# Kernel optimization log

Measured on AMD Instinct MI355X. Metric: run time of the kernel, lower is better.

The kernel has to match this reference:

```python
import jax, jax.numpy as jnp
import numpy as np

DIM = 128
BATCH = 262144
N_PAIRS = DIM * (DIM - 1) // 2  # 8128

# Static pair ordering exactly as in the torch module: (i, j) for i in range(dim) for j in range(i+1, dim)
_p = np.array([(i, j) for i in range(DIM) for j in range(i + 1, DIM)], dtype=np.int32)
I_IDX = jnp.asarray(_p[:, 0])
J_IDX = jnp.asarray(_p[:, 1])


def setup_inputs() -> dict:
    key = jax.random.key(0)
    k1, k2 = jax.random.split(key)
    x = jax.random.normal(k1, (BATCH, DIM), dtype=jnp.float32)
    angles = jax.random.normal(k2, (N_PAIRS,), dtype=jnp.float32) * 0.01
    bias = jnp.zeros((DIM,), dtype=jnp.float32)
    return {"x": x, "angles": angles, "bias": bias}


def _rotation_matrix(angles):
    # The layer is linear: applying the ordered Givens sweep to every row of x
    # equals x @ W where W is the sweep applied to eye(dim) (cf. weight_matrix()).
    # Building W via a scan over the 8128 rotations is the efficient faithful form.
    cos, sin = jnp.cos(angles), jnp.sin(angles)

    def step(W, vals):
        i, j, c, s = vals
        wi = W[:, i]  # [dim]
        wj = W[:, j]
        # out[:, [i,j]] @ [[c, -s], [s, c]]  ->  new_i = wi*c + wj*s ; new_j = wj*c - wi*s
        W = W.at[:, i].set(wi * c + wj * s)
        W = W.at[:, j].set(wj * c - wi * s)
        return W, None

    W0 = jnp.eye(DIM, dtype=angles.dtype)
    W, _ = jax.lax.scan(step, W0, (I_IDX, J_IDX, cos, sin))
    return W


def reference(x, angles, bias):
    W = _rotation_matrix(angles)  # [dim, dim] orthogonal
    return x @ W + bias
```

## Files before the change

kernel.cpp:

```cpp
#include <hip/hip_runtime.h>

typedef float  floatx4  __attribute__((ext_vector_type(4)));
typedef short  bf16x8   __attribute__((ext_vector_type(8)));
typedef float  facc4    __attribute__((ext_vector_type(4)));

__device__ __forceinline__ unsigned short f2bf(float f) {
  unsigned u = __builtin_bit_cast(unsigned, f);
  u = u + 0x7fffu + ((u >> 16) & 1u);
  return (unsigned short)(u >> 16);
}

template <int I0, int I1>
__device__ void gen_chunk(const float* __restrict__ ang, float* __restrict__ out,
                          float* lcs, int tid) {
  constexpr int P0 = I0 * 127 - I0 * (I0 - 1) / 2;
  constexpr int P1 = I1 * 127 - I1 * (I1 - 1) / 2;
  constexpr int NROT = P1 - P0;
  for (int idx = tid; idx < NROT; idx += 256) {
    float s, c;
    sincosf(ang[P0 + idx], &s, &c);
    lcs[2 * idx] = c;
    lcs[2 * idx + 1] = s;
  }
  __syncthreads();
  if (tid >= 128) return;
  float w[128];
#pragma unroll
  for (int k = 0; k < 128; ++k) w[k] = (k == tid) ? 1.0f : 0.0f;
#pragma unroll
  for (int i = I0; i < I1; ++i) {
    float wi = w[i];
#pragma unroll
    for (int j = i + 1; j < 128; ++j) {
      const int p = (i * 127 - (i * (i - 1)) / 2 + (j - i - 1)) - P0;
      const float2 cs2 = *(const float2*)(&lcs[2 * p]);
      const float c = cs2.x, s = cs2.y;
      const float wj = w[j];
      w[j] = fmaf(wj, c, -(wi * s));
      wi   = fmaf(wj, s, wi * c);
    }
    w[i] = wi;
  }
  floatx4* o = (floatx4*)(out + (size_t)tid * 128);
#pragma unroll
  for (int k = 0; k < 32; ++k) {
    floatx4 v;
    v[0] = w[4 * k]; v[1] = w[4 * k + 1]; v[2] = w[4 * k + 2]; v[3] = w[4 * k + 3];
    o[k] = v;
  }
}

__global__ __launch_bounds__(256) void k_wgen(const float* __restrict__ ang,
                                              float* __restrict__ out) {
  __shared__ float lcs[2144];
  const int tid = threadIdx.x;
  switch (blockIdx.x) {
    case 0:  gen_chunk<0,   8>(ang, out + 0 * 16384, lcs, tid); break;
    case 1:  gen_chunk<8,  17>(ang, out + 1 * 16384, lcs, tid); break;
    case 2:  gen_chunk<17, 27>(ang, out + 2 * 16384, lcs, tid); break;
    case 3:  gen_chunk<27, 37>(ang, out + 3 * 16384, lcs, tid); break;
    case 4:  gen_chunk<37, 49>(ang, out + 4 * 16384, lcs, tid); break;
    case 5:  gen_chunk<49, 64>(ang, out + 5 * 16384, lcs, tid); break;
    case 6:  gen_chunk<64, 82>(ang, out + 6 * 16384, lcs, tid); break;
    default: gen_chunk<82, 127>(ang, out + 7 * 16384, lcs, tid); break;
  }
}

__global__ __launch_bounds__(128) void k_combine(const float* __restrict__ chunks,
                                                 unsigned short* __restrict__ wt) {
  __shared__ float sv[128];
  const int r = blockIdx.x;
  const int t = threadIdx.x;
  float v = chunks[r * 128 + t];
  for (int m = 1; m < 8; ++m) {
    __syncthreads();
    sv[t] = v;
    __syncthreads();
    const float* Cm = chunks + m * 16384 + t;
    float a0 = 0.f, a1 = 0.f, a2 = 0.f, a3 = 0.f;
#pragma unroll
    for (int k = 0; k < 128; k += 4) {
      a0 = fmaf(sv[k],     Cm[(k)     * 128], a0);
      a1 = fmaf(sv[k + 1], Cm[(k + 1) * 128], a1);
      a2 = fmaf(sv[k + 2], Cm[(k + 2) * 128], a2);
      a3 = fmaf(sv[k + 3], Cm[(k + 3) * 128], a3);
    }
    v = (a0 + a1) + (a2 + a3);
  }
  wt[t * 136 + r] = f2bf(v);
}

__global__ __launch_bounds__(256) void k_gemm(const float* __restrict__ x,
                                              const unsigned short* __restrict__ wt,
                                              const float* __restrict__ bias,
                                              float* __restrict__ y) {
  __shared__ unsigned short sW[128 * 136];
  __shared__ float sB[128];
  const int tid = threadIdx.x;
  {
    const floatx4* src = (const floatx4*)wt;
    floatx4* dst = (floatx4*)sW;
#pragma unroll
    for (int i2 = 0; i2 < 9; ++i2) {
      int idx = tid + i2 * 256;
      if (idx < 2176) dst[idx] = src[idx];
    }
    if (tid < 128) sB[tid] = bias[tid];
  }
  __syncthreads();

  const int wave = tid >> 6, lane = tid & 63;
  const int m16 = lane & 15, h = lane >> 4;

  const size_t row0 = (size_t)blockIdx.x * 256 + wave * 64 + m16;
  const float* xr0 = x + row0 * 128;
  float* yr0 = y + row0 * 128;

  floatx4 a[8];
#pragma unroll
  for (int c = 0; c < 4; ++c) {
    a[2 * c]     = *(const floatx4*)(xr0 + c * 32 + h * 8);
    a[2 * c + 1] = *(const floatx4*)(xr0 + c * 32 + h * 8 + 4);
  }

#pragma unroll
  for (int it = 0; it < 4; ++it) {
    bf16x8 af[4];
#pragma unroll
    for (int c = 0; c < 4; ++c) {
#pragma unroll
      for (int q = 0; q < 8; ++q) {
        const float f = (q < 4) ? a[2 * c][q] : a[2 * c + 1][q - 4];
        af[c][q] = (short)f2bf(f);
      }
    }
    if (it < 3) {
      const float* xr = xr0 + (size_t)(it + 1) * 16 * 128;
#pragma unroll
      for (int c = 0; c < 4; ++c) {
        a[2 * c]     = *(const floatx4*)(xr + c * 32 + h * 8);
        a[2 * c + 1] = *(const floatx4*)(xr + c * 32 + h * 8 + 4);
      }
    }
    facc4 acc[8];
#pragma unroll
    for (int t = 0; t < 8; ++t) acc[t] = *(const facc4*)(sB + t * 16 + h * 4);
#pragma unroll
    for (int c = 0; c < 4; ++c) {
#pragma unroll
      for (int t = 0; t < 8; ++t) {
        const bf16x8 bw = *(const bf16x8*)(&sW[(t * 16 + m16) * 136 + c * 32 + h * 8]);
        acc[t] = __builtin_amdgcn_mfma_f32_16x16x32_bf16(bw, af[c], acc[t], 0, 0, 0);
      }
    }
    float* yr = yr0 + (size_t)it * 16 * 128;
#pragma unroll
    for (int t = 0; t < 8; ++t) {
      *(floatx4*)(yr + t * 16 + h * 4) = acc[t];
    }
  }
}

extern "C" void kernel_launch(void* const* d_in, const int* in_sizes, int n_in,
                              void* d_out, int out_size, void* d_ws, size_t ws_size,
                              hipStream_t stream) {
  const float* x    = (const float*)d_in[0];
  const float* ang  = (const float*)d_in[1];
  const float* bias = (const float*)d_in[2];
  float* y = (float*)d_out;

  char* ws = (char*)d_ws;
  float* chunks      = (float*)ws;
  unsigned short* wt = (unsigned short*)(ws + 524288);

  k_wgen   <<<8,    256, 0, stream>>>(ang, chunks);
  k_combine<<<128,  128, 0, stream>>>(chunks, wt);
  k_gemm   <<<1024, 256, 0, stream>>>(x, wt, bias, y);
}
```

Baseline: 287.7 us.

## Restructure GEMM: register-resident W slices, shared bf16 X tiles, staged coalesced stores

Each wave now keeps its 32-column slice of W in registers and reuses it across 16 row tiles. X tiles are loaded coalesced, converted to bf16 and placed in a double-buffered, XOR-swizzled shared buffer with global prefetch two tiles ahead. Outputs go through a swizzled shared transpose so global stores are coalesced. This removes the per-block 34KB W copy into shared memory and the strided per-lane X loads, at the cost of a block-wide barrier per tile.

```diff
diff --git a/kernel.cpp b/kernel.cpp
--- a/kernel.cpp
+++ b/kernel.cpp
@@ -3,6 +3,7 @@
 typedef float  floatx4  __attribute__((ext_vector_type(4)));
 typedef short  bf16x8   __attribute__((ext_vector_type(8)));
 typedef float  facc4    __attribute__((ext_vector_type(4)));
+typedef unsigned short ushortx4 __attribute__((ext_vector_type(4)));
 
 __device__ __forceinline__ unsigned short f2bf(float f) {
   unsigned u = __builtin_bit_cast(unsigned, f);
@@ -90,74 +91,102 @@
   wt[t * 136 + r] = f2bf(v);
 }
 
-__global__ __launch_bounds__(256) void k_gemm(const float* __restrict__ x,
-                                              const unsigned short* __restrict__ wt,
-                                              const float* __restrict__ bias,
-                                              float* __restrict__ y) {
-  __shared__ unsigned short sW[128 * 136];
-  __shared__ float sB[128];
+__global__ __launch_bounds__(256, 4) void k_gemm(const float* __restrict__ x,
+                                                 const unsigned short* __restrict__ wt,
+                                                 const float* __restrict__ bias,
+                                                 float* __restrict__ y) {
+  __shared__ unsigned short sX[2][2048];
+  __shared__ float sT[4][512];
+
   const int tid = threadIdx.x;
+  const int wv = tid >> 6, lane = tid & 63;
+  const int m16 = lane & 15, h = lane >> 4;
+
+  bf16x8 bw[2][4];
+#pragma unroll
+  for (int t = 0; t < 2; ++t)
+#pragma unroll
+    for (int c = 0; c < 4; ++c)
+      bw[t][c] = *(const bf16x8*)(wt + (size_t)(wv * 32 + t * 16 + m16) * 136
+                                     + c * 32 + h * 8);
+  facc4 bfr[2];
+#pragma unroll
+  for (int t = 0; t < 2; ++t)
+    bfr[t] = *(const facc4*)(bias + wv * 32 + t * 16 + h * 4);
+
+  const float* xb = x + (size_t)blockIdx.x * 256 * 128;
+  float*       yb = y + (size_t)blockIdx.x * 256 * 128;
+
+  const int r0 = tid >> 5;
+  const int c0 = (tid & 31) * 4;
+  const unsigned sw0  = (unsigned)((r0 & 7) << 4);
+  const unsigned stb0 = (unsigned)(r0 * 256 + ((c0 * 2) ^ sw0));
+  const unsigned stb1 = stb0 + 2048;
+
+  floatx4 pA0 = *(const floatx4*)(xb + tid * 4);
+  floatx4 pA1 = *(const floatx4*)(xb + 1024 + tid * 4);
+  floatx4 pB0 = *(const floatx4*)(xb + 2048 + tid * 4);
+  floatx4 pB1 = *(const floatx4*)(xb + 3072 + tid * 4);
   {
-    const floatx4* src = (const floatx4*)wt;
-    floatx4* dst = (floatx4*)sW;
-#pragma unroll
-    for (int i2 = 0; i2 < 9; ++i2) {
-      int idx = tid + i2 * 256;
-      if (idx < 2176) dst[idx] = src[idx];
-    }
-    if (tid < 128) sB[tid] = bias[tid];
+    ushortx4 q0, q1;
+#pragma unroll
+    for (int q = 0; q < 4; ++q) { q0[q] = f2bf(pA0[q]); q1[q] = f2bf(pA1[q]); }
+    *(ushortx4*)((char*)&sX[0][0] + stb0) = q0;
+    *(ushortx4*)((char*)&sX[0][0] + stb1) = q1;
   }
   __syncthreads();
 
-  const int wave = tid >> 6, lane = tid & 63;
-  const int m16 = lane & 15, h = lane >> 4;
-
-  const size_t row0 = (size_t)blockIdx.x * 256 + wave * 64 + m16;
-  const float* xr0 = x + row0 * 128;
-  float* yr0 = y + row0 * 128;
-
-  floatx4 a[8];
-#pragma unroll
-  for (int c = 0; c < 4; ++c) {
-    a[2 * c]     = *(const floatx4*)(xr0 + c * 32 + h * 8);
-    a[2 * c + 1] = *(const floatx4*)(xr0 + c * 32 + h * 8 + 4);
-  }
-
-#pragma unroll
-  for (int it = 0; it < 4; ++it) {
+#pragma unroll
+  for (int it = 0; it < 16; ++it) {
+    const int cur = it & 1;
     bf16x8 af[4];
 #pragma unroll
+    for (int c = 0; c < 4; ++c)
+      af[c] = *(const bf16x8*)((const char*)&sX[cur][0] +
+               (unsigned)(m16 * 256 + ((c * 64 + h * 16) ^ ((m16 & 7) << 4))));
+
+    if (it + 2 < 16) {
+      const float* s2 = xb + (size_t)(it + 2) * 2048;
+      if (cur == 0) {
+        pA0 = *(const floatx4*)(s2 + tid * 4);
+        pA1 = *(const floatx4*)(s2 + 1024 + tid * 4);
+      } else {
+        pB0 = *(const floatx4*)(s2 + tid * 4);
+        pB1 = *(const floatx4*)(s2 + 1024 + tid * 4);
+      }
+    }
+    if (it + 1 < 16) {
+      ushortx4 q0, q1;
+      if (cur == 0) {
+#pragma unroll
+        for (int q = 0; q < 4; ++q) { q0[q] = f2bf(pB0[q]); q1[q] = f2bf(pB1[q]); }
+      } else {
+#pragma unroll
+        for (int q = 0; q < 4; ++q) { q0[q] = f2bf(pA0[q]); q1[q] = f2bf(pA1[q]); }
+      }
+      *(ushortx4*)((char*)&sX[cur ^ 1][0] + stb0) = q0;
+      *(ushortx4*)((char*)&sX[cur ^ 1][0] + stb1) = q1;
+    }
+
+    facc4 acc0 = bfr[0], acc1 = bfr[1];
+#pragma unroll
     for (int c = 0; c < 4; ++c) {
-#pragma unroll
-      for (int q = 0; q < 8; ++q) {
-        const float f = (q < 4) ? a[2 * c][q] : a[2 * c + 1][q - 4];
-        af[c][q] = (short)f2bf(f);
-      }
-    }
-    if (it < 3) {
-      const float* xr = xr0 + (size_t)(it + 1) * 16 * 128;
-#pragma unroll
-      for (int c = 0; c < 4; ++c) {
-        a[2 * c]     = *(const floatx4*)(xr + c * 32 + h * 8);
-        a[2 * c + 1] = *(const floatx4*)(xr + c * 32 + h * 8 + 4);
-      }
-    }
-    facc4 acc[8];
-#pragma unroll
-    for (int t = 0; t < 8; ++t) acc[t] = *(const facc4*)(sB + t * 16 + h * 4);
-#pragma unroll
-    for (int c = 0; c < 4; ++c) {
-#pragma unroll
-      for (int t = 0; t < 8; ++t) {
-        const bf16x8 bw = *(const bf16x8*)(&sW[(t * 16 + m16) * 136 + c * 32 + h * 8]);
-        acc[t] = __builtin_amdgcn_mfma_f32_16x16x32_bf16(bw, af[c], acc[t], 0, 0, 0);
-      }
-    }
-    float* yr = yr0 + (size_t)it * 16 * 128;
-#pragma unroll
-    for (int t = 0; t < 8; ++t) {
-      *(floatx4*)(yr + t * 16 + h * 4) = acc[t];
-    }
+      acc0 = __builtin_amdgcn_mfma_f32_16x16x32_bf16(bw[0][c], af[c], acc0, 0, 0, 0);
+      acc1 = __builtin_amdgcn_mfma_f32_16x16x32_bf16(bw[1][c], af[c], acc1, 0, 0, 0);
+    }
+
+    *(floatx4*)((char*)&sT[wv][0] +
+        (unsigned)(m16 * 128 + ((h * 16)      ^ ((m16 & 7) << 4)))) = acc0;
+    *(floatx4*)((char*)&sT[wv][0] +
+        (unsigned)(m16 * 128 + ((64 + h * 16) ^ ((m16 & 7) << 4)))) = acc1;
+#pragma unroll
+    for (int s = 0; s < 2; ++s) {
+      const int row = s * 8 + (lane >> 3);
+      floatx4 v = *(const floatx4*)((const char*)&sT[wv][0] +
+                  (unsigned)(row * 128 + (((lane & 7) * 16) ^ ((row & 7) << 4))));
+      *(floatx4*)(yb + (size_t)(it * 16 + row) * 128 + wv * 32 + (lane & 7) * 4) = v;
+    }
+    __syncthreads();
   }
 }
 
```

Result: no change. 287.5 us (-0.1%).
